# Kernel optimization log

Hardware: AMD Instinct MI355X
Metric: run time of the kernel (lower is better)

Reference implementation:

```python
import jax, jax.numpy as jnp
import numpy as np


def setup_inputs() -> dict:
    key = jax.random.key(0)
    ks = jax.random.split(key, 8)
    B, S, Nc, C, Cseed = 4, 4096, 8192, 512, 256
    return {
        "query_xyz": jax.random.normal(ks[0], (B, S, 3), dtype=jnp.float32),
        "ref_xyz": jax.random.normal(ks[1], (B, Nc, 3), dtype=jnp.float32),
        "ref_feat": jax.random.normal(ks[2], (B, C, Nc), dtype=jnp.float32),
        "seed_features": jax.random.normal(ks[3], (B, Cseed, S), dtype=jnp.float32),
        "W_seed_proj": jax.random.normal(ks[4], (Cseed, C), dtype=jnp.float32) * 0.02,
        "b_seed_proj": jax.random.normal(ks[5], (Cseed,), dtype=jnp.float32) * 0.02,
        "W_concat_proj": jax.random.normal(ks[6], (Cseed, 2 * Cseed), dtype=jnp.float32) * 0.02,
        "b_concat_proj": jax.random.normal(ks[7], (Cseed,), dtype=jnp.float32) * 0.02,
    }


def _nn_gather(query_xyz, ref_xyz, ref_feat):
    # torch.cdist(p=2) + argmin: argmin over squared distance is identical
    # (sqrt is monotonic), so we skip the sqrt.
    q2 = jnp.sum(query_xyz * query_xyz, axis=-1, keepdims=True)      # (B,S,1)
    r2 = jnp.sum(ref_xyz * ref_xyz, axis=-1)[:, None, :]             # (B,1,Nc)
    qr = jnp.einsum("bsd,bnd->bsn", query_xyz, ref_xyz)              # (B,S,Nc)
    d2 = q2 + r2 - 2.0 * qr                                          # (B,S,Nc)
    idx = jnp.argmin(d2, axis=-1)                                    # (B,S) int
    # gather nearest-neighbor features: (B,C,Nc) -> (B,C,S)
    return jnp.take_along_axis(ref_feat, idx[:, None, :], axis=2)


def reference(query_xyz, ref_xyz, ref_feat, seed_features,
              W_seed_proj, b_seed_proj, W_concat_proj, b_concat_proj):
    lift3d_raw = _nn_gather(query_xyz, ref_xyz, ref_feat)            # (B,C,S)
    # 1x1 Conv1d == channel matmul
    lift3d_seed = jnp.einsum("oc,bcs->bos", W_seed_proj, lift3d_raw) \
                  + b_seed_proj[None, :, None]                       # (B,256,S)
    fused = jnp.concatenate([seed_features, lift3d_seed], axis=1)    # (B,512,S)
    out = jnp.einsum("oc,bcs->bos", W_concat_proj, fused) \
          + b_concat_proj[None, :, None]                             # (B,256,S)
    return out
```

## Files before the change

kernel.cpp:

```cpp
#include <hip/hip_runtime.h>

#define B_   4
#define S_   4096
#define NC   8192
#define C_   512
#define CS   256
#define KTOT 768

typedef __attribute__((ext_vector_type(8))) short short8;
typedef __attribute__((ext_vector_type(4))) float f32x4;

static __device__ __forceinline__ unsigned short f2bf(float x) {
    unsigned u = __builtin_bit_cast(unsigned, x);
    unsigned r = u + 0x7FFFu + ((u >> 16) & 1u);
    return (unsigned short)(r >> 16);
}

__global__ __launch_bounds__(256) void prep_kernel(
        const float* __restrict__ rxyz, float4* __restrict__ refpk,
        const float* __restrict__ Wcat, const float* __restrict__ Wseed,
        unsigned short* __restrict__ Wcomb,
        const float* __restrict__ bseed, const float* __restrict__ bcat,
        float* __restrict__ beff) {
    __shared__ float sa[64][68];
    __shared__ float sbt[64][68];
    int bid = blockIdx.x;
    int tid = threadIdx.x;

    if (bid < 64) {
        int w = tid >> 6, l = tid & 63;
        int o = bid * 4 + w;
        float4 wv = *(const float4*)(Wcat + (size_t)o * 512 + 256 + l * 4);
        float4 bb = *(const float4*)(bseed + l * 4);
        float acc = __fmul_rn(wv.x, bb.x);
        acc = fmaf(wv.y, bb.y, acc);
        acc = fmaf(wv.z, bb.z, acc);
        acc = fmaf(wv.w, bb.w, acc);
        #pragma unroll
        for (int off = 32; off > 0; off >>= 1) acc += __shfl_down(acc, off);
        if (l == 0) beff[o] = acc + bcat[o];
    } else if (bid < 96) {
        int xb = bid - 64;
        int tc = (xb & 7) * 64;
        int to = (xb >> 3) * 64;
        int tx = tid & 15, ty = tid >> 4;
        float acc[4][4] = {};
        for (int kt = 0; kt < 256; kt += 64) {
            __syncthreads();
            #pragma unroll
            for (int r = 0; r < 4; ++r) {
                int oo = r * 16 + ty;
                float4 v = *(const float4*)(Wcat + (size_t)(to + oo) * 512 + 256 + kt + tx * 4);
                sa[oo][tx * 4 + 0] = v.x;
                sa[oo][tx * 4 + 1] = v.y;
                sa[oo][tx * 4 + 2] = v.z;
                sa[oo][tx * 4 + 3] = v.w;
                float4 u = *(const float4*)(Wseed + (size_t)(kt + oo) * 512 + tc + tx * 4);
                sbt[oo][tx * 4 + 0] = u.x;
                sbt[oo][tx * 4 + 1] = u.y;
                sbt[oo][tx * 4 + 2] = u.z;
                sbt[oo][tx * 4 + 3] = u.w;
            }
            __syncthreads();
            for (int k = 0; k < 64; ++k) {
                float a[4], bb2[4];
                #pragma unroll
                for (int i = 0; i < 4; ++i) a[i] = sa[ty * 4 + i][k];
                #pragma unroll
                for (int j = 0; j < 4; ++j) bb2[j] = sbt[k][tx * 4 + j];
                #pragma unroll
                for (int i = 0; i < 4; ++i)
                    #pragma unroll
                    for (int j = 0; j < 4; ++j)
                        acc[i][j] = fmaf(a[i], bb2[j], acc[i][j]);
            }
        }
        #pragma unroll
        for (int i = 0; i < 4; ++i)
            #pragma unroll
            for (int j = 0; j < 4; ++j)
                Wcomb[(size_t)(to + ty * 4 + i) * KTOT + 256 + tc + tx * 4 + j] = f2bf(acc[i][j]);
    } else if (bid < 160) {
        int g = ((bid - 96) * 256 + tid) * 4;
        int o = g >> 8, cc = g & 255;
        float4 v = *(const float4*)(Wcat + (size_t)o * 512 + cc);
        ushort4 ov;
        ov.x = f2bf(v.x); ov.y = f2bf(v.y); ov.z = f2bf(v.z); ov.w = f2bf(v.w);
        *(ushort4*)(Wcomb + (size_t)o * KTOT + cc) = ov;
    } else {
        int gid = (bid - 160) * 256 + tid;
        float x = rxyz[gid * 3 + 0];
        float y = rxyz[gid * 3 + 1];
        float z = rxyz[gid * 3 + 2];
        float r2 = __fadd_rn(__fadd_rn(__fmul_rn(x, x), __fmul_rn(y, y)), __fmul_rn(z, z));
        refpk[gid] = make_float4(x, y, z, r2);
    }
}

__global__ __launch_bounds__(256, 4) void mid_kernel(
        const float* __restrict__ qxyz, const float4* __restrict__ refpk,
        float* __restrict__ pval, int* __restrict__ pidx,
        const float* __restrict__ rf, unsigned short* __restrict__ refT,
        const float* __restrict__ seed, unsigned short* __restrict__ seedT) {
    __shared__ float t[64][65];
    int bid = blockIdx.x;
    int tid = threadIdx.x;
    int r7 = bid % 7;
    int g7 = bid / 7;

    if (r7 == 0 || r7 == 4) {
        int aid = g7 * 2 + (r7 == 4);
        int sblk = aid & 127;
        int c = (aid >> 7) & 3;
        int b = aid >> 9;
        int lane = tid & 63;
        int qg = tid >> 6;
        int sbase = sblk * 32 + qg * 8;

        float qx[8], qy[8], qz[8], q2[8];
        #pragma unroll
        for (int q = 0; q < 8; ++q) {
            const float* qp = qxyz + ((size_t)(b * S_ + sbase + q)) * 3;
            qx[q] = qp[0]; qy[q] = qp[1]; qz[q] = qp[2];
            q2[q] = __fadd_rn(__fadd_rn(__fmul_rn(qx[q], qx[q]), __fmul_rn(qy[q], qy[q])),
                              __fmul_rn(qz[q], qz[q]));
        }

        const float4* ep = refpk + (size_t)b * NC + c * 2048 + lane;
        float best[8];
        int bj[8];
        #pragma unroll
        for (int q = 0; q < 8; ++q) { best[q] = 3.4028235e38f; bj[q] = 0; }

        float4 r0 = ep[0];
        float4 r1 = ep[64];
        #pragma unroll 2
        for (int j = 0; j < 32; j += 2) {
            float4 r2 = r0, r3 = r1;
            if (j + 2 < 32) {
                r2 = ep[(j + 2) * 64];
                r3 = ep[(j + 3) * 64];
            }
            #pragma unroll
            for (int q = 0; q < 8; ++q) {
                float qr = __fadd_rn(__fadd_rn(__fmul_rn(qx[q], r0.x), __fmul_rn(qy[q], r0.y)),
                                     __fmul_rn(qz[q], r0.z));
                float s = __fadd_rn(q2[q], r0.w);
                float d2 = fmaf(qr, -2.0f, s);
                if (d2 < best[q]) { best[q] = d2; bj[q] = j; }
            }
            #pragma unroll
            for (int q = 0; q < 8; ++q) {
                float qr = __fadd_rn(__fadd_rn(__fmul_rn(qx[q], r1.x), __fmul_rn(qy[q], r1.y)),
                                     __fmul_rn(qz[q], r1.z));
                float s = __fadd_rn(q2[q], r1.w);
                float d2 = fmaf(qr, -2.0f, s);
                if (d2 < best[q]) { best[q] = d2; bj[q] = j + 1; }
            }
            r0 = r2;
            r1 = r3;
        }

        int bx[8];
        #pragma unroll
        for (int q = 0; q < 8; ++q) bx[q] = c * 2048 + bj[q] * 64 + lane;

        #pragma unroll
        for (int m = 1; m < 64; m <<= 1) {
            #pragma unroll
            for (int q = 0; q < 8; ++q) {
                float vv = __shfl_xor(best[q], m, 64);
                int xx = __shfl_xor(bx[q], m, 64);
                if (vv < best[q] || (vv == best[q] && xx < bx[q])) {
                    best[q] = vv; bx[q] = xx;
                }
            }
        }
        if (lane == 0) {
            #pragma unroll
            for (int q = 0; q < 8; ++q) {
                int qs = b * S_ + sbase + q;
                pval[qs * 4 + c] = best[q];
                pidx[qs * 4 + c] = bx[q];
            }
        }
    } else if (r7 != 6) {
        int id = g7 * 4 + (r7 - 1 - (r7 > 4 ? 1 : 0));
        int b = id >> 10;
        int c0 = ((id >> 7) & 7) * 64;
        int n0 = (id & 127) * 64;
        int tx = tid & 15, ty = tid >> 4;
        #pragma unroll
        for (int r = 0; r < 4; ++r) {
            int cc = r * 16 + ty;
            float4 v = *(const float4*)(rf + ((size_t)b * C_ + c0 + cc) * NC + n0 + tx * 4);
            t[tx * 4 + 0][cc] = v.x;
            t[tx * 4 + 1][cc] = v.y;
            t[tx * 4 + 2][cc] = v.z;
            t[tx * 4 + 3][cc] = v.w;
        }
        __syncthreads();
        #pragma unroll
        for (int r = 0; r < 4; ++r) {
            int n = r * 16 + ty;
            ushort4 o;
            o.x = f2bf(t[n][tx * 4 + 0]);
            o.y = f2bf(t[n][tx * 4 + 1]);
            o.z = f2bf(t[n][tx * 4 + 2]);
            o.w = f2bf(t[n][tx * 4 + 3]);
            *(ushort4*)(refT + ((size_t)b * NC + n0 + n) * C_ + c0 + tx * 4) = o;
        }
    } else {
        int id = g7;
        int b = id >> 8;
        int rem = id & 255;
        int c0 = (rem >> 6) * 64;
        int s0 = (rem & 63) * 64;
        int tx = tid & 15, ty = tid >> 4;
        #pragma unroll
        for (int r = 0; r < 4; ++r) {
            int cc = r * 16 + ty;
            float4 v = *(const float4*)(seed + ((size_t)b * CS + c0 + cc) * S_ + s0 + tx * 4);
            t[tx * 4 + 0][cc] = v.x;
            t[tx * 4 + 1][cc] = v.y;
            t[tx * 4 + 2][cc] = v.z;
            t[tx * 4 + 3][cc] = v.w;
        }
        __syncthreads();
        #pragma unroll
        for (int r = 0; r < 4; ++r) {
            int n = r * 16 + ty;
            ushort4 o;
            o.x = f2bf(t[n][tx * 4 + 0]);
            o.y = f2bf(t[n][tx * 4 + 1]);
            o.z = f2bf(t[n][tx * 4 + 2]);
            o.w = f2bf(t[n][tx * 4 + 3]);
            *(ushort4*)(seedT + ((size_t)b * S_ + s0 + n) * CS + c0 + tx * 4) = o;
        }
    }
}

__global__ __launch_bounds__(256, 2) void fused_gemm_kernel(
        const unsigned short* __restrict__ Wcomb,
        const unsigned short* __restrict__ seedT,
        const unsigned short* __restrict__ refT,
        const float* __restrict__ pval,
        const int* __restrict__ pidx,
        const float* __restrict__ beff,
        float* __restrict__ out) {
    __shared__ __align__(16) unsigned short sA[2][64][72];
    __shared__ __align__(16) unsigned short sB[2][128][72];
    __shared__ int sIdx[128];
    __shared__ float sBias[64];

    int tid = threadIdx.x;
    int b = blockIdx.z;
    int m0 = blockIdx.y * 64;
    int s0 = blockIdx.x * 128;
    if (tid < 128) {
        int qs = b * S_ + s0 + tid;
        float v = pval[qs * 4 + 0];
        int x = pidx[qs * 4 + 0];
        #pragma unroll
        for (int c = 1; c < 4; ++c) {
            float vv = pval[qs * 4 + c];
            int xx = pidx[qs * 4 + c];
            if (vv < v || (vv == v && xx < x)) { v = vv; x = xx; }
        }
        sIdx[tid] = x & (NC - 1);
        if (tid < 64) sBias[tid] = beff[m0 + tid];
    }

    int lane = tid & 63;
    int w = tid >> 6;
    int wm = w >> 1;
    int wn = w & 1;
    int ln = lane & 15;
    int quad = lane >> 4;
    int q8 = quad * 8;

    int mmA  = tid >> 2;
    int kk16 = (tid & 3) << 4;
    int nB   = tid >> 1;
    int kk32 = (tid & 1) << 5;
    const unsigned short* Arow = Wcomb + (size_t)(m0 + mmA) * KTOT + kk16;
    const unsigned short* Srow = seedT + ((size_t)b * S_ + s0 + nB) * CS + kk32;

    f32x4 acc[2][4];
    #pragma unroll
    for (int i = 0; i < 2; ++i)
        #pragma unroll
        for (int j = 0; j < 4; ++j)
            acc[i][j] = (f32x4){0.f, 0.f, 0.f, 0.f};

    short8 ra0, ra1, rb0, rb1, rb2, rb3;

    #define SLOAD(PK) do {                                                         \
        int pk0 = (PK) * 64;                                                       \
        ra0 = *(const short8*)(Arow + pk0);                                        \
        ra1 = *(const short8*)(Arow + pk0 + 8);                                    \
        const unsigned short* Brow =                                               \
            (pk0 < 256) ? (Srow + pk0)                                             \
                        : (refT + ((size_t)b * NC + sIdx[nB]) * C_                 \
                           + (pk0 - 256) + kk32);                                  \
        rb0 = *(const short8*)(Brow);                                              \
        rb1 = *(const short8*)(Brow + 8);                                          \
        rb2 = *(const short8*)(Brow + 16);                                         \
        rb3 = *(const short8*)(Brow + 24);                                         \
    } while (0)

    #define SWRITE(BUF) do {                                                       \
        *(short8*)&sA[BUF][mmA][kk16]      = ra0;                                  \
        *(short8*)&sA[BUF][mmA][kk16 + 8]  = ra1;                                  \
        *(short8*)&sB[BUF][nB][kk32]       = rb0;                                  \
        *(short8*)&sB[BUF][nB][kk32 + 8]   = rb1;                                  \
        *(short8*)&sB[BUF][nB][kk32 + 16]  = rb2;                                  \
        *(short8*)&sB[BUF][nB][kk32 + 24]  = rb3;                                  \
    } while (0)

    SLOAD(0);
    SWRITE(0);
    __syncthreads();

    int cur = 0;
    for (int ks = 0; ks < 12; ++ks) {
        if (ks < 11) SLOAD(ks + 1);
        #pragma unroll
        for (int kf = 0; kf < 2; ++kf) {
            short8 af[2], bfr[4];
            #pragma unroll
            for (int i = 0; i < 2; ++i)
                af[i] = *(const short8*)&sA[cur][wm * 32 + i * 16 + ln][kf * 32 + q8];
            #pragma unroll
            for (int j = 0; j < 4; ++j)
                bfr[j] = *(const short8*)&sB[cur][wn * 64 + j * 16 + ln][kf * 32 + q8];
            #pragma unroll
            for (int i = 0; i < 2; ++i)
                #pragma unroll
                for (int j = 0; j < 4; ++j)
                    acc[i][j] = __builtin_amdgcn_mfma_f32_16x16x32_bf16(af[i], bfr[j], acc[i][j], 0, 0, 0);
        }
        if (ks < 11) {
            SWRITE(cur ^ 1);
            __syncthreads();
            cur ^= 1;
        }
    }
    #undef SLOAD
    #undef SWRITE

    #pragma unroll
    for (int i = 0; i < 2; ++i) {
        int mb = wm * 32 + i * 16 + quad * 4;
        #pragma unroll
        for (int j = 0; j < 4; ++j) {
            int col = s0 + wn * 64 + j * 16 + ln;
            #pragma unroll
            for (int r = 0; r < 4; ++r) {
                int m = mb + r;
                out[((size_t)b * CS + m0 + m) * S_ + col] = acc[i][j][r] + sBias[m];
            }
        }
    }
}

extern "C" void kernel_launch(void* const* d_in, const int* in_sizes, int n_in,
                              void* d_out, int out_size, void* d_ws, size_t ws_size,
                              hipStream_t stream) {
    const float* qxyz  = (const float*)d_in[0];
    const float* rxyz  = (const float*)d_in[1];
    const float* rfeat = (const float*)d_in[2];
    const float* seed  = (const float*)d_in[3];
    const float* Wseed = (const float*)d_in[4];
    const float* bseed = (const float*)d_in[5];
    const float* Wcat  = (const float*)d_in[6];
    const float* bcat  = (const float*)d_in[7];
    float* out = (float*)d_out;

    char* ws = (char*)d_ws;
    float* pval           = (float*)(ws);
    int* pidx             = (int*)(ws + 262144);
    float* beff           = (float*)(ws + 524288);
    float4* refpk         = (float4*)(ws + 528384);
    unsigned short* Wcomb = (unsigned short*)(ws + 1052672);
    unsigned short* refT  = (unsigned short*)(ws + 1445888);
    unsigned short* seedT = (unsigned short*)(ws + 35000320);

    hipLaunchKernelGGL(prep_kernel, dim3(288), dim3(256), 0, stream,
                       rxyz, refpk, Wcat, Wseed, Wcomb, bseed, bcat, beff);
    hipLaunchKernelGGL(mid_kernel, dim3(7168), dim3(256), 0, stream,
                       qxyz, refpk, pval, pidx, rfeat, refT, seed, seedT);
    hipLaunchKernelGGL(fused_gemm_kernel, dim3(32, 4, 4), dim3(256), 0, stream,
                       Wcomb, seedT, refT, pval, pidx, beff, out);
}
```

Baseline: 181.4 us.

## Fuse ref-feature transpose tiles into NN-search blocks to overlap memory with compute

Each nearest-neighbour search block now also transposes one tile of ref_feat to bf16. It issues the global loads before the distance loop so the memory latency hides behind the ALU-bound search. The grid shrinks from 7168 to 5120 blocks, and the remaining ref tiles and the seed tiles are handled by the other blocks. The cost is more register pressure in the search blocks (four held float4s) and a less even mix of work per block.

```diff
diff --git a/kernel.cpp b/kernel.cpp
--- a/kernel.cpp
+++ b/kernel.cpp
@@ -105,11 +105,20 @@
     __shared__ float t[64][65];
     int bid = blockIdx.x;
     int tid = threadIdx.x;
-    int r7 = bid % 7;
-    int g7 = bid / 7;
-
-    if (r7 == 0 || r7 == 4) {
-        int aid = g7 * 2 + (r7 == 4);
+    int r5 = bid % 5;
+    int g5 = bid / 5;
+
+    if (r5 == 0 || r5 == 2) {
+        int aid = g5 * 2 + (r5 == 2);
+        int bt  = aid >> 10;
+        int tc0 = ((aid >> 7) & 7) * 64;
+        int tn0 = (aid & 127) * 64;
+        int tx = tid & 15, ty = tid >> 4;
+        float4 tv[4];
+        #pragma unroll
+        for (int r = 0; r < 4; ++r)
+            tv[r] = *(const float4*)(rf + ((size_t)bt * C_ + tc0 + r * 16 + ty) * NC + tn0 + tx * 4);
+
         int sblk = aid & 127;
         int c = (aid >> 7) & 3;
         int b = aid >> 9;
@@ -184,20 +193,14 @@
                 pidx[qs * 4 + c] = bx[q];
             }
         }
-    } else if (r7 != 6) {
-        int id = g7 * 4 + (r7 - 1 - (r7 > 4 ? 1 : 0));
-        int b = id >> 10;
-        int c0 = ((id >> 7) & 7) * 64;
-        int n0 = (id & 127) * 64;
-        int tx = tid & 15, ty = tid >> 4;
+
         #pragma unroll
         for (int r = 0; r < 4; ++r) {
             int cc = r * 16 + ty;
-            float4 v = *(const float4*)(rf + ((size_t)b * C_ + c0 + cc) * NC + n0 + tx * 4);
-            t[tx * 4 + 0][cc] = v.x;
-            t[tx * 4 + 1][cc] = v.y;
-            t[tx * 4 + 2][cc] = v.z;
-            t[tx * 4 + 3][cc] = v.w;
+            t[tx * 4 + 0][cc] = tv[r].x;
+            t[tx * 4 + 1][cc] = tv[r].y;
+            t[tx * 4 + 2][cc] = tv[r].z;
+            t[tx * 4 + 3][cc] = tv[r].w;
         }
         __syncthreads();
         #pragma unroll
@@ -208,34 +211,63 @@
             o.y = f2bf(t[n][tx * 4 + 1]);
             o.z = f2bf(t[n][tx * 4 + 2]);
             o.w = f2bf(t[n][tx * 4 + 3]);
-            *(ushort4*)(refT + ((size_t)b * NC + n0 + n) * C_ + c0 + tx * 4) = o;
+            *(ushort4*)(refT + ((size_t)bt * NC + tn0 + n) * C_ + tc0 + tx * 4) = o;
         }
     } else {
-        int id = g7;
-        int b = id >> 8;
-        int rem = id & 255;
-        int c0 = (rem >> 6) * 64;
-        int s0 = (rem & 63) * 64;
+        int j3 = (r5 == 1) ? 0 : ((r5 == 3) ? 1 : 2);
+        int pid = g5 * 3 + j3;
         int tx = tid & 15, ty = tid >> 4;
-        #pragma unroll
-        for (int r = 0; r < 4; ++r) {
-            int cc = r * 16 + ty;
-            float4 v = *(const float4*)(seed + ((size_t)b * CS + c0 + cc) * S_ + s0 + tx * 4);
-            t[tx * 4 + 0][cc] = v.x;
-            t[tx * 4 + 1][cc] = v.y;
-            t[tx * 4 + 2][cc] = v.z;
-            t[tx * 4 + 3][cc] = v.w;
-        }
-        __syncthreads();
-        #pragma unroll
-        for (int r = 0; r < 4; ++r) {
-            int n = r * 16 + ty;
-            ushort4 o;
-            o.x = f2bf(t[n][tx * 4 + 0]);
-            o.y = f2bf(t[n][tx * 4 + 1]);
-            o.z = f2bf(t[n][tx * 4 + 2]);
-            o.w = f2bf(t[n][tx * 4 + 3]);
-            *(ushort4*)(seedT + ((size_t)b * S_ + s0 + n) * CS + c0 + tx * 4) = o;
+        if (pid < 2048) {
+            int id = 2048 + pid;
+            int b = id >> 10;
+            int c0 = ((id >> 7) & 7) * 64;
+            int n0 = (id & 127) * 64;
+            #pragma unroll
+            for (int r = 0; r < 4; ++r) {
+                int cc = r * 16 + ty;
+                float4 v = *(const float4*)(rf + ((size_t)b * C_ + c0 + cc) * NC + n0 + tx * 4);
+                t[tx * 4 + 0][cc] = v.x;
+                t[tx * 4 + 1][cc] = v.y;
+                t[tx * 4 + 2][cc] = v.z;
+                t[tx * 4 + 3][cc] = v.w;
+            }
+            __syncthreads();
+            #pragma unroll
+            for (int r = 0; r < 4; ++r) {
+                int n = r * 16 + ty;
+                ushort4 o;
+                o.x = f2bf(t[n][tx * 4 + 0]);
+                o.y = f2bf(t[n][tx * 4 + 1]);
+                o.z = f2bf(t[n][tx * 4 + 2]);
+                o.w = f2bf(t[n][tx * 4 + 3]);
+                *(ushort4*)(refT + ((size_t)b * NC + n0 + n) * C_ + c0 + tx * 4) = o;
+            }
+        } else {
+            int id = pid - 2048;
+            int b = id >> 8;
+            int rem = id & 255;
+            int c0 = (rem >> 6) * 64;
+            int s0 = (rem & 63) * 64;
+            #pragma unroll
+            for (int r = 0; r < 4; ++r) {
+                int cc = r * 16 + ty;
+                float4 v = *(const float4*)(seed + ((size_t)b * CS + c0 + cc) * S_ + s0 + tx * 4);
+                t[tx * 4 + 0][cc] = v.x;
+                t[tx * 4 + 1][cc] = v.y;
+                t[tx * 4 + 2][cc] = v.z;
+                t[tx * 4 + 3][cc] = v.w;
+            }
+            __syncthreads();
+            #pragma unroll
+            for (int r = 0; r < 4; ++r) {
+                int n = r * 16 + ty;
+                ushort4 o;
+                o.x = f2bf(t[n][tx * 4 + 0]);
+                o.y = f2bf(t[n][tx * 4 + 1]);
+                o.z = f2bf(t[n][tx * 4 + 2]);
+                o.w = f2bf(t[n][tx * 4 + 3]);
+                *(ushort4*)(seedT + ((size_t)b * S_ + s0 + n) * CS + c0 + tx * 4) = o;
+            }
         }
     }
 }
@@ -388,7 +420,7 @@
 
     hipLaunchKernelGGL(prep_kernel, dim3(288), dim3(256), 0, stream,
                        rxyz, refpk, Wcat, Wseed, Wcomb, bseed, bcat, beff);
-    hipLaunchKernelGGL(mid_kernel, dim3(7168), dim3(256), 0, stream,
+    hipLaunchKernelGGL(mid_kernel, dim3(5120), dim3(256), 0, stream,
                        qxyz, refpk, pval, pidx, rfeat, refT, seed, seedT);
     hipLaunchKernelGGL(fused_gemm_kernel, dim3(32, 4, 4), dim3(256), 0, stream,
                        Wcomb, seedT, refT, pval, pidx, beff, out);
```

New measurement: 184.6 us. About the same (+1.8%).

## Merge argmin and transpose work into persistent-style blocks with alternating order

Applied to the files above, without the earlier changes.

Restructures mid_kernel from 7168 blocks, each doing one role, into 1024 blocks that each do two argmin chunks and five transpose tiles. Alternate groups of 256 blocks run compute-bound argmin first or memory-bound transposes first, so ALU and memory phases overlap across the GPU. This cuts block launch overhead and mixes the two workloads per CU. The risk is fewer blocks and longer serial work per block, which could hurt latency hiding and tail balance.

```diff
diff --git a/kernel.cpp b/kernel.cpp
--- a/kernel.cpp
+++ b/kernel.cpp
@@ -97,99 +97,96 @@
     }
 }
 
-__global__ __launch_bounds__(256, 4) void mid_kernel(
+static __device__ __forceinline__ void argmin_chunk(
+        int aid, int tid,
         const float* __restrict__ qxyz, const float4* __restrict__ refpk,
-        float* __restrict__ pval, int* __restrict__ pidx,
+        float* __restrict__ pval, int* __restrict__ pidx) {
+    int sblk = aid & 127;
+    int c = (aid >> 7) & 3;
+    int b = aid >> 9;
+    int lane = tid & 63;
+    int qg = tid >> 6;
+    int sbase = sblk * 32 + qg * 8;
+
+    float qx[8], qy[8], qz[8], q2[8];
+    #pragma unroll
+    for (int q = 0; q < 8; ++q) {
+        const float* qp = qxyz + ((size_t)(b * S_ + sbase + q)) * 3;
+        qx[q] = qp[0]; qy[q] = qp[1]; qz[q] = qp[2];
+        q2[q] = __fadd_rn(__fadd_rn(__fmul_rn(qx[q], qx[q]), __fmul_rn(qy[q], qy[q])),
+                          __fmul_rn(qz[q], qz[q]));
+    }
+
+    const float4* ep = refpk + (size_t)b * NC + c * 2048 + lane;
+    float best[8];
+    int bj[8];
+    #pragma unroll
+    for (int q = 0; q < 8; ++q) { best[q] = 3.4028235e38f; bj[q] = 0; }
+
+    float4 r0 = ep[0];
+    float4 r1 = ep[64];
+    #pragma unroll 2
+    for (int j = 0; j < 32; j += 2) {
+        float4 r2 = r0, r3 = r1;
+        if (j + 2 < 32) {
+            r2 = ep[(j + 2) * 64];
+            r3 = ep[(j + 3) * 64];
+        }
+        #pragma unroll
+        for (int q = 0; q < 8; ++q) {
+            float qr = __fadd_rn(__fadd_rn(__fmul_rn(qx[q], r0.x), __fmul_rn(qy[q], r0.y)),
+                                 __fmul_rn(qz[q], r0.z));
+            float s = __fadd_rn(q2[q], r0.w);
+            float d2 = fmaf(qr, -2.0f, s);
+            if (d2 < best[q]) { best[q] = d2; bj[q] = j; }
+        }
+        #pragma unroll
+        for (int q = 0; q < 8; ++q) {
+            float qr = __fadd_rn(__fadd_rn(__fmul_rn(qx[q], r1.x), __fmul_rn(qy[q], r1.y)),
+                                 __fmul_rn(qz[q], r1.z));
+            float s = __fadd_rn(q2[q], r1.w);
+            float d2 = fmaf(qr, -2.0f, s);
+            if (d2 < best[q]) { best[q] = d2; bj[q] = j + 1; }
+        }
+        r0 = r2;
+        r1 = r3;
+    }
+
+    int bx[8];
+    #pragma unroll
+    for (int q = 0; q < 8; ++q) bx[q] = c * 2048 + bj[q] * 64 + lane;
+
+    #pragma unroll
+    for (int m = 1; m < 64; m <<= 1) {
+        #pragma unroll
+        for (int q = 0; q < 8; ++q) {
+            float vv = __shfl_xor(best[q], m, 64);
+            int xx = __shfl_xor(bx[q], m, 64);
+            if (vv < best[q] || (vv == best[q] && xx < bx[q])) {
+                best[q] = vv; bx[q] = xx;
+            }
+        }
+    }
+    if (lane == 0) {
+        #pragma unroll
+        for (int q = 0; q < 8; ++q) {
+            int qs = b * S_ + sbase + q;
+            pval[qs * 4 + c] = best[q];
+            pidx[qs * 4 + c] = bx[q];
+        }
+    }
+}
+
+static __device__ __forceinline__ void transpose_tile(
+        int id, int tid, float (*t)[65],
         const float* __restrict__ rf, unsigned short* __restrict__ refT,
         const float* __restrict__ seed, unsigned short* __restrict__ seedT) {
-    __shared__ float t[64][65];
-    int bid = blockIdx.x;
-    int tid = threadIdx.x;
-    int r7 = bid % 7;
-    int g7 = bid / 7;
-
-    if (r7 == 0 || r7 == 4) {
-        int aid = g7 * 2 + (r7 == 4);
-        int sblk = aid & 127;
-        int c = (aid >> 7) & 3;
-        int b = aid >> 9;
-        int lane = tid & 63;
-        int qg = tid >> 6;
-        int sbase = sblk * 32 + qg * 8;
-
-        float qx[8], qy[8], qz[8], q2[8];
-        #pragma unroll
-        for (int q = 0; q < 8; ++q) {
-            const float* qp = qxyz + ((size_t)(b * S_ + sbase + q)) * 3;
-            qx[q] = qp[0]; qy[q] = qp[1]; qz[q] = qp[2];
-            q2[q] = __fadd_rn(__fadd_rn(__fmul_rn(qx[q], qx[q]), __fmul_rn(qy[q], qy[q])),
-                              __fmul_rn(qz[q], qz[q]));
-        }
-
-        const float4* ep = refpk + (size_t)b * NC + c * 2048 + lane;
-        float best[8];
-        int bj[8];
-        #pragma unroll
-        for (int q = 0; q < 8; ++q) { best[q] = 3.4028235e38f; bj[q] = 0; }
-
-        float4 r0 = ep[0];
-        float4 r1 = ep[64];
-        #pragma unroll 2
-        for (int j = 0; j < 32; j += 2) {
-            float4 r2 = r0, r3 = r1;
-            if (j + 2 < 32) {
-                r2 = ep[(j + 2) * 64];
-                r3 = ep[(j + 3) * 64];
-            }
-            #pragma unroll
-            for (int q = 0; q < 8; ++q) {
-                float qr = __fadd_rn(__fadd_rn(__fmul_rn(qx[q], r0.x), __fmul_rn(qy[q], r0.y)),
-                                     __fmul_rn(qz[q], r0.z));
-                float s = __fadd_rn(q2[q], r0.w);
-                float d2 = fmaf(qr, -2.0f, s);
-                if (d2 < best[q]) { best[q] = d2; bj[q] = j; }
-            }
-            #pragma unroll
-            for (int q = 0; q < 8; ++q) {
-                float qr = __fadd_rn(__fadd_rn(__fmul_rn(qx[q], r1.x), __fmul_rn(qy[q], r1.y)),
-                                     __fmul_rn(qz[q], r1.z));
-                float s = __fadd_rn(q2[q], r1.w);
-                float d2 = fmaf(qr, -2.0f, s);
-                if (d2 < best[q]) { best[q] = d2; bj[q] = j + 1; }
-            }
-            r0 = r2;
-            r1 = r3;
-        }
-
-        int bx[8];
-        #pragma unroll
-        for (int q = 0; q < 8; ++q) bx[q] = c * 2048 + bj[q] * 64 + lane;
-
-        #pragma unroll
-        for (int m = 1; m < 64; m <<= 1) {
-            #pragma unroll
-            for (int q = 0; q < 8; ++q) {
-                float vv = __shfl_xor(best[q], m, 64);
-                int xx = __shfl_xor(bx[q], m, 64);
-                if (vv < best[q] || (vv == best[q] && xx < bx[q])) {
-                    best[q] = vv; bx[q] = xx;
-                }
-            }
-        }
-        if (lane == 0) {
-            #pragma unroll
-            for (int q = 0; q < 8; ++q) {
-                int qs = b * S_ + sbase + q;
-                pval[qs * 4 + c] = best[q];
-                pidx[qs * 4 + c] = bx[q];
-            }
-        }
-    } else if (r7 != 6) {
-        int id = g7 * 4 + (r7 - 1 - (r7 > 4 ? 1 : 0));
+    int tx = tid & 15, ty = tid >> 4;
+    __syncthreads();
+    if (id < 4096) {
         int b = id >> 10;
         int c0 = ((id >> 7) & 7) * 64;
         int n0 = (id & 127) * 64;
-        int tx = tid & 15, ty = tid >> 4;
         #pragma unroll
         for (int r = 0; r < 4; ++r) {
             int cc = r * 16 + ty;
@@ -211,12 +208,11 @@
             *(ushort4*)(refT + ((size_t)b * NC + n0 + n) * C_ + c0 + tx * 4) = o;
         }
     } else {
-        int id = g7;
-        int b = id >> 8;
-        int rem = id & 255;
+        int sid = id - 4096;
+        int b = sid >> 8;
+        int rem = sid & 255;
         int c0 = (rem >> 6) * 64;
         int s0 = (rem & 63) * 64;
-        int tx = tid & 15, ty = tid >> 4;
         #pragma unroll
         for (int r = 0; r < 4; ++r) {
             int cc = r * 16 + ty;
@@ -237,6 +233,29 @@
             o.w = f2bf(t[n][tx * 4 + 3]);
             *(ushort4*)(seedT + ((size_t)b * S_ + s0 + n) * CS + c0 + tx * 4) = o;
         }
+    }
+}
+
+__global__ __launch_bounds__(256, 4) void mid_kernel(
+        const float* __restrict__ qxyz, const float4* __restrict__ refpk,
+        float* __restrict__ pval, int* __restrict__ pidx,
+        const float* __restrict__ rf, unsigned short* __restrict__ refT,
+        const float* __restrict__ seed, unsigned short* __restrict__ seedT) {
+    __shared__ float t[64][65];
+    int g = blockIdx.x;
+    int tid = threadIdx.x;
+    bool scanFirst = ((g >> 8) & 1) == 0;
+
+    if (scanFirst) {
+        argmin_chunk(2 * g,     tid, qxyz, refpk, pval, pidx);
+        argmin_chunk(2 * g + 1, tid, qxyz, refpk, pval, pidx);
+        for (int tt = 0; tt < 5; ++tt)
+            transpose_tile(g * 5 + tt, tid, t, rf, refT, seed, seedT);
+    } else {
+        for (int tt = 0; tt < 5; ++tt)
+            transpose_tile(g * 5 + tt, tid, t, rf, refT, seed, seedT);
+        argmin_chunk(2 * g,     tid, qxyz, refpk, pval, pidx);
+        argmin_chunk(2 * g + 1, tid, qxyz, refpk, pval, pidx);
     }
 }
 
@@ -388,7 +407,7 @@
 
     hipLaunchKernelGGL(prep_kernel, dim3(288), dim3(256), 0, stream,
                        rxyz, refpk, Wcat, Wseed, Wcomb, bseed, bcat, beff);
-    hipLaunchKernelGGL(mid_kernel, dim3(7168), dim3(256), 0, stream,
+    hipLaunchKernelGGL(mid_kernel, dim3(1024), dim3(256), 0, stream,
                        qxyz, refpk, pval, pidx, rfeat, refT, seed, seedT);
     hipLaunchKernelGGL(fused_gemm_kernel, dim3(32, 4, 4), dim3(256), 0, stream,
                        Wcomb, seedT, refT, pval, pidx, beff, out);
```

Measured after the change: 182.0 us. No clear change (+0.3%).
